# Performance work log

Measured on AMD Instinct MI355X. Metric: run time of the kernel, lower is better.

The kernel has to match this reference:

```python
import jax, jax.numpy as jnp
import numpy as np

N = 500_000      # nodes
E = 4_000_000    # edges (avg degree 8)
F_IN = 24        # n_input (includeHeading=False, coords=False)
H = 64           # n_hidden
K = 6            # K_block Chebyshev order
OUT = 6          # n_output
EPS = 1e-5       # BatchNorm eps


def setup_inputs() -> dict:
    key = jax.random.key(0)
    ks = jax.random.split(key, 8)
    x = jax.random.normal(ks[0], (N, F_IN), dtype=jnp.float32)
    edge_index = jax.random.randint(ks[1], (2, E), 0, N, dtype=jnp.int32)
    # ChebConv(24 -> 64, K=6): stacked per-order weights [K, F_IN, H] + bias
    W1 = jax.random.normal(ks[2], (K, F_IN, H), dtype=jnp.float32) * (1.0 / np.sqrt(F_IN))
    b1 = jnp.zeros((H,), dtype=jnp.float32)
    # BatchNorm1d(64) affine params
    gamma = jnp.ones((H,), dtype=jnp.float32)
    beta = jnp.zeros((H,), dtype=jnp.float32)
    # conv_mix ChebConv(64 -> 6, K=1)
    Wmix = jax.random.normal(ks[3], (1, H, OUT), dtype=jnp.float32) * (1.0 / np.sqrt(H))
    bmix = jnp.zeros((OUT,), dtype=jnp.float32)
    return {"x": x, "edge_index": edge_index, "W1": W1, "b1": b1,
            "gamma": gamma, "beta": beta, "Wmix": Wmix, "bmix": bmix}


def cheb_conv(x, edge_index, W, b):
    """PyG ChebConv with normalization='sym', lambda_max=2.
    L_hat = L - I = -D^{-1/2} A D^{-1/2} (zero diagonal).
    """
    Kk = W.shape[0]
    row, col = edge_index[0], edge_index[1]  # messages flow row -> col
    deg = jax.ops.segment_sum(jnp.ones((E,), x.dtype), col, num_segments=N)
    dis = jnp.where(deg > 0, jax.lax.rsqrt(jnp.maximum(deg, 1.0)), 0.0)
    norm = -(dis[row] * dis[col])  # [E]

    def prop(h):  # h: [N, F] -> L_hat @ h via gather-scale-scatter
        return jax.ops.segment_sum(norm[:, None] * h[row], col, num_segments=N)

    Tx0 = x
    out = Tx0 @ W[0]
    if Kk > 1:
        Tx1 = prop(Tx0)
        out = out + Tx1 @ W[1]
        for k in range(2, Kk):
            Tx2 = 2.0 * prop(Tx1) - Tx0
            out = out + Tx2 @ W[k]
            Tx0, Tx1 = Tx1, Tx2
    return out + b


def reference(x, edge_index, W1, b1, gamma, beta, Wmix, bmix):
    # Kipfblock: ChebConv -> BatchNorm1d (batch stats) -> ReLU
    h = cheb_conv(x, edge_index, W1, b1)            # [N, H]
    mean = jnp.mean(h, axis=0)
    var = jnp.mean(jnp.square(h - mean), axis=0)    # biased var, as torch BN training
    h = (h - mean) * jax.lax.rsqrt(var + EPS) * gamma + beta
    h = jax.nn.relu(h)
    # conv_mix: ChebConv K=1 reduces to a dense linear (T_0 = x only)
    y = h @ Wmix[0] + bmix                          # [N, OUT]
    # F.dropout is identity in eval mode
    return y
```

## Files before the change

### kernel.cpp

```cpp
#include <hip/hip_runtime.h>
#include <hip/hip_fp16.h>

#define NN 500000
#define NE 4000000
#define FI 24
#define FH 64
#define KC 6
#define FO 6
#define BN_EPS 1e-5f

#define SLOTS 32
#define RH 32
#define NMT (NN / 16)
#define PASS_GRID 1024

#define EPT 8
#define CHUNK (256 * EPT)
#define NCHUNK ((NE + CHUNK - 1) / CHUNK)

#define BUCKETS 512
#define BW 977
#define BCAP 15500

#define RMASK 0x7FFFFu

typedef _Float16 half8 __attribute__((ext_vector_type(8)));
typedef float f32x4 __attribute__((ext_vector_type(4)));
typedef int int4v __attribute__((ext_vector_type(4)));
union U4H8 { uint4 u; half8 h; };


__device__ __forceinline__ void acc8(float* a, float d, uint4 u) {
    const __half2* h2 = (const __half2*)&u;
    #pragma unroll
    for (int j = 0; j < 4; ++j) {
        float2 f = __half22float2(h2[j]);
        a[2 * j]     += d * f.x;
        a[2 * j + 1] += d * f.y;
    }
}

__device__ __forceinline__ uint4 pack8(const float* a) {
    uint4 u;
    __half2* h2 = (__half2*)&u;
    #pragma unroll
    for (int j = 0; j < 4; ++j) h2[j] = __floats2half2_rn(a[2 * j], a[2 * j + 1]);
    return u;
}


__global__ __launch_bounds__(256) void k_scatter(
    const int* __restrict__ row, const int* __restrict__ col,
    unsigned int* __restrict__ ebuf, int* __restrict__ cur) {
    __shared__ unsigned int val[CHUNK];
    __shared__ unsigned short bk[CHUNK];
    __shared__ int hist[BUCKETS], base[BUCKETS], rk[BUCKETS];
    for (int t = threadIdx.x; t < BUCKETS; t += 256) { hist[t] = 0; rk[t] = 0; }
    __syncthreads();
    const int b0 = blockIdx.x * CHUNK;
    #pragma unroll
    for (int i = 0; i < EPT / 4; ++i) {
        int li4 = (i * 256 + threadIdx.x) * 4;
        int e0 = b0 + li4;
        if (e0 + 4 <= NE) {
            int4v c4 = *(const int4v*)(col + e0);
            int4v r4 = *(const int4v*)(row + e0);
            #pragma unroll
            for (int j = 0; j < 4; ++j) {
                int c = c4[j], r = r4[j];
                int b = c / BW, cl = c - b * BW;
                val[li4 + j] = (unsigned int)r | ((unsigned int)cl << 19);
                bk[li4 + j] = (unsigned short)b;
                atomicAdd(&hist[b], 1);
            }
        } else {
            for (int j = 0; j < 4; ++j) {
                int e = e0 + j, li = li4 + j;
                if (e < NE) {
                    int c = col[e], r = row[e];
                    int b = c / BW, cl = c - b * BW;
                    val[li] = (unsigned int)r | ((unsigned int)cl << 19);
                    bk[li] = (unsigned short)b;
                    atomicAdd(&hist[b], 1);
                } else {
                    bk[li] = 0xFFFF;
                }
            }
        }
    }
    __syncthreads();
    for (int t = threadIdx.x; t < BUCKETS; t += 256) {
        int n = hist[t];
        base[t] = n ? atomicAdd(&cur[t], n) : 0;
    }
    __syncthreads();
    #pragma unroll
    for (int i = 0; i < EPT / 4; ++i) {
        int li4 = (i * 256 + threadIdx.x) * 4;
        #pragma unroll
        for (int j = 0; j < 4; ++j) {
            int li = li4 + j;
            int b = bk[li];
            if (b != 0xFFFF) {
                int rkk = atomicAdd(&rk[b], 1);
                int pos = base[b] + rkk;
                if (pos < BCAP) ebuf[(size_t)b * BCAP + pos] = val[li];
            }
        }
    }
}


__global__ __launch_bounds__(256) void k_build(
    const unsigned int* __restrict__ ebuf, const int* __restrict__ cur,
    int* __restrict__ cnt, int* __restrict__ csrcT) {
    __shared__ int cl_cnt[BW];
    const int b = blockIdx.x;
    const int nbase = b * BW;
    const int width = (NN - nbase < BW) ? (NN - nbase) : BW;
    for (int i = threadIdx.x; i < BW; i += 256) cl_cnt[i] = 0;
    __syncthreads();
    int nb = cur[b];
    if (nb > BCAP) nb = BCAP;
    for (int i = threadIdx.x; i < nb; i += 256) {
        unsigned int v = ebuf[(size_t)b * BCAP + i];
        int cl = v >> 19;
        int r = v & RMASK;
        int pos = atomicAdd(&cl_cnt[cl], 1);
        if (pos < SLOTS) csrcT[(size_t)pos * NN + nbase + cl] = r;
    }
    __syncthreads();
    for (int i = threadIdx.x; i < width; i += 256) cnt[nbase + i] = cl_cnt[i];
}

__global__ void k_dis(const int* __restrict__ cnt, float* __restrict__ dis) {
    int n = blockIdx.x * blockDim.x + threadIdx.x;
    if (n < NN) {
        int d = cnt[n];
        dis[n] = d > 0 ? rsqrtf((float)d) : 0.0f;
    }
}


__global__ __launch_bounds__(256) void k_pack(
    const int* __restrict__ cnt, unsigned int* __restrict__ csrcT) {
    int n = blockIdx.x * 256 + threadIdx.x;
    if (n >= NN) return;
    int deg = cnt[n];
    if (deg > SLOTS) deg = SLOTS;
    for (int s = 0; s < deg; ++s) {
        size_t idx = (size_t)s * NN + n;
        unsigned int r = csrcT[idx] & RMASK;
        int dg = cnt[r];
        if (dg > 8191) dg = 8191;
        csrcT[idx] = r | ((unsigned int)dg << 19);
    }
}


__global__ void k_xhalf(const float* __restrict__ x, __half* __restrict__ Th0) {
    int n = blockIdx.x * blockDim.x + threadIdx.x;
    if (n >= NN) return;
    const float* r = x + (size_t)n * FI;
    float v[24];
    #pragma unroll
    for (int i = 0; i < 6; ++i) {
        float4 f = ((const float4*)r)[i];
        v[4 * i] = f.x; v[4 * i + 1] = f.y; v[4 * i + 2] = f.z; v[4 * i + 3] = f.w;
    }
    uint4* o = (uint4*)(Th0 + (size_t)n * RH);
    o[0] = pack8(v); o[1] = pack8(v + 8); o[2] = pack8(v + 16);
    o[3] = make_uint4(0, 0, 0, 0);
}


template<bool FIRST>
__global__ __launch_bounds__(256) void k_prop(
    const int* __restrict__ cnt, const unsigned int* __restrict__ csrcT,
    const float* __restrict__ dis,
    const __half* __restrict__ Tin, const __half* __restrict__ Tpp,
    __half* __restrict__ Tout) {
    int t = blockIdx.x * 256 + threadIdx.x;
    int n = t >> 1, half = t & 1;
    if (n >= NN) return;
    int deg = cnt[n];
    if (deg > SLOTS) deg = SLOTS;
    float a[24];
    #pragma unroll
    for (int j = 0; j < 24; ++j) a[j] = 0.0f;
    int s = half;
    for (; s + 2 < deg; s += 4) {
        unsigned int e0 = csrcT[(size_t)s * NN + n];
        unsigned int e1 = csrcT[(size_t)(s + 2) * NN + n];
        const uint4* p0 = (const uint4*)(Tin + (size_t)(e0 & RMASK) * RH);
        const uint4* p1 = (const uint4*)(Tin + (size_t)(e1 & RMASK) * RH);
        uint4 u00 = p0[0], u01 = p0[1], u02 = p0[2];
        uint4 u10 = p1[0], u11 = p1[1], u12 = p1[2];
        unsigned int g0 = e0 >> 19, g1 = e1 >> 19;
        float d0 = g0 ? rsqrtf((float)g0) : 0.0f;
        float d1 = g1 ? rsqrtf((float)g1) : 0.0f;
        acc8(a, d0, u00); acc8(a + 8, d0, u01); acc8(a + 16, d0, u02);
        acc8(a, d1, u10); acc8(a + 8, d1, u11); acc8(a + 16, d1, u12);
    }
    if (s < deg) {
        unsigned int e0 = csrcT[(size_t)s * NN + n];
        unsigned int g0 = e0 >> 19;
        float d0 = g0 ? rsqrtf((float)g0) : 0.0f;
        const uint4* p0 = (const uint4*)(Tin + (size_t)(e0 & RMASK) * RH);
        acc8(a, d0, p0[0]); acc8(a + 8, d0, p0[1]); acc8(a + 16, d0, p0[2]);
    }
    #pragma unroll
    for (int j = 0; j < 24; ++j) a[j] += __shfl_xor(a[j], 1);
    float local[16];
    #pragma unroll
    for (int j = 0; j < 16; ++j) {
        float ev = a[j];
        float od = (j < 8) ? a[16 + j] : 0.0f;
        local[j] = half ? od : ev;
    }
    float m = FIRST ? -dis[n] : -2.0f * dis[n];
    if (FIRST) {
        #pragma unroll
        for (int j = 0; j < 16; ++j) local[j] *= m;
    } else {
        const uint4* pr = (const uint4*)(Tpp + (size_t)n * RH) + half * 2;
        uint4 q0 = pr[0], q1 = pr[1];
        float pv[16];
        {
            const __half2* h2 = (const __half2*)&q0;
            #pragma unroll
            for (int j = 0; j < 4; ++j) { float2 f = __half22float2(h2[j]); pv[2*j] = f.x; pv[2*j+1] = f.y; }
        }
        {
            const __half2* h2 = (const __half2*)&q1;
            #pragma unroll
            for (int j = 0; j < 4; ++j) { float2 f = __half22float2(h2[j]); pv[8+2*j] = f.x; pv[8+2*j+1] = f.y; }
        }
        #pragma unroll
        for (int j = 0; j < 16; ++j) local[j] = m * local[j] - pv[j];
    }
    uint4* o = (uint4*)(Tout + (size_t)n * RH) + half * 2;
    o[0] = pack8(local); o[1] = pack8(local + 8);
}


__device__ __forceinline__ void build_bfrags(const float* __restrict__ W1, uint4* Bf) {
    for (int s = threadIdx.x; s < KC * 4 * 64; s += 256) {
        int lane = s & 63, blk = s >> 6;
        int seg = blk >> 2, nb = blk & 3;
        int q = lane >> 4, n = lane & 15;
        float v[8];
        #pragma unroll
        for (int j = 0; j < 8; ++j) {
            int k = q * 8 + j;
            v[j] = (k < FI) ? W1[(seg * FI + k) * FH + nb * 16 + n] : 0.0f;
        }
        U4H8 u;
        __half2* h2 = (__half2*)&u;
        #pragma unroll
        for (int j = 0; j < 4; ++j) h2[j] = __floats2half2_rn(v[2 * j], v[2 * j + 1]);
        Bf[s] = u.u;
    }
}

__global__ __launch_bounds__(256) void k_pass1(
    const __half* __restrict__ Th, const float* __restrict__ W1,
    const float* __restrict__ b1, float* __restrict__ stats,
    __half* __restrict__ h) {
    __shared__ uint4 Bf[KC * 4 * 64];
    __shared__ float st[2 * FH];
    build_bfrags(W1, Bf);
    if (threadIdx.x < 2 * FH) st[threadIdx.x] = 0.0f;
    __syncthreads();
    const int lane = threadIdx.x & 63;
    const int q = lane >> 4, ln = lane & 15;
    const int wid = blockIdx.x * 4 + (threadIdx.x >> 6);
    const int nw = gridDim.x * 4;
    float bias[4];
    #pragma unroll
    for (int nb = 0; nb < 4; ++nb) bias[nb] = b1[nb * 16 + ln];
    float ssum[4] = {0, 0, 0, 0}, sqsum[4] = {0, 0, 0, 0};
    for (int t = wid; t < NMT; t += nw) {
        const int n0 = t * 16;
        f32x4 acc[4];
        #pragma unroll
        for (int nb = 0; nb < 4; ++nb)
            acc[nb] = (f32x4){bias[nb], bias[nb], bias[nb], bias[nb]};
        #pragma unroll
        for (int seg = 0; seg < KC; ++seg) {
            U4H8 a;
            a.u = *(const uint4*)(Th + (size_t)seg * ((size_t)NN * RH)
                                  + (size_t)(n0 + ln) * RH + q * 8);
            #pragma unroll
            for (int nb = 0; nb < 4; ++nb) {
                U4H8 b; b.u = Bf[(seg * 4 + nb) * 64 + lane];
                acc[nb] = __builtin_amdgcn_mfma_f32_16x16x32_f16(a.h, b.h, acc[nb], 0, 0, 0);
            }
        }
        #pragma unroll
        for (int nb = 0; nb < 4; ++nb) {
            #pragma unroll
            for (int r = 0; r < 4; ++r) {
                float v = acc[nb][r];
                ssum[nb] += v;
                sqsum[nb] += v * v;
                h[(size_t)(n0 + q * 4 + r) * FH + nb * 16 + ln] = __float2half(v);
            }
        }
    }
    #pragma unroll
    for (int nb = 0; nb < 4; ++nb) {
        ssum[nb]  += __shfl_xor(ssum[nb], 16);  ssum[nb]  += __shfl_xor(ssum[nb], 32);
        sqsum[nb] += __shfl_xor(sqsum[nb], 16); sqsum[nb] += __shfl_xor(sqsum[nb], 32);
    }
    if (lane < 16) {
        #pragma unroll
        for (int nb = 0; nb < 4; ++nb) {
            atomicAdd(&st[nb * 16 + ln], ssum[nb]);
            atomicAdd(&st[FH + nb * 16 + ln], sqsum[nb]);
        }
    }
    __syncthreads();
    if (threadIdx.x < 2 * FH) atomicAdd(&stats[threadIdx.x], st[threadIdx.x]);
}

__global__ void k_finalize(const float* __restrict__ stats, const float* __restrict__ gamma,
                           const float* __restrict__ beta, float* __restrict__ ss) {
    int f = threadIdx.x;
    if (f < FH) {
        float mean = stats[f] * (1.0f / NN);
        float var  = stats[f + FH] * (1.0f / NN) - mean * mean;
        float rstd = rsqrtf(var + BN_EPS);
        float sc = gamma[f] * rstd;
        ss[f] = sc;
        ss[f + FH] = beta[f] - mean * sc;
    }
}


__global__ __launch_bounds__(256) void k_pass2(
    const __half* __restrict__ h, const float* __restrict__ ss,
    const float* __restrict__ Wmix, const float* __restrict__ bmix,
    float* __restrict__ y) {
    __shared__ float tab[FH * 8];
    for (int f = threadIdx.x; f < FH; f += 256) {
        tab[f * 8 + 0] = ss[f];
        tab[f * 8 + 1] = ss[FH + f];
        #pragma unroll
        for (int o = 0; o < FO; ++o) tab[f * 8 + 2 + o] = Wmix[f * FO + o];
    }
    __syncthreads();
    int n = blockIdx.x * 256 + threadIdx.x;
    if (n >= NN) return;
    const uint4* hr = (const uint4*)(h + (size_t)n * FH);
    float p[FO];
    #pragma unroll
    for (int o = 0; o < FO; ++o) p[o] = bmix[o];
    #pragma unroll
    for (int blk = 0; blk < 8; ++blk) {
        U4H8 u; u.u = hr[blk];
        const __half2* h2 = (const __half2*)&u;
        #pragma unroll
        for (int j = 0; j < 4; ++j) {
            float2 f2 = __half22float2(h2[j]);
            int f = blk * 8 + j * 2;
            {
                float4 t0 = *(const float4*)&tab[f * 8];
                float4 t1 = *(const float4*)&tab[f * 8 + 4];
                float hv = fmaxf(f2.x * t0.x + t0.y, 0.0f);
                p[0] += hv * t0.z; p[1] += hv * t0.w;
                p[2] += hv * t1.x; p[3] += hv * t1.y;
                p[4] += hv * t1.z; p[5] += hv * t1.w;
            }
            {
                float4 t0 = *(const float4*)&tab[(f + 1) * 8];
                float4 t1 = *(const float4*)&tab[(f + 1) * 8 + 4];
                float hv = fmaxf(f2.y * t0.x + t0.y, 0.0f);
                p[0] += hv * t0.z; p[1] += hv * t0.w;
                p[2] += hv * t1.x; p[3] += hv * t1.y;
                p[4] += hv * t1.z; p[5] += hv * t1.w;
            }
        }
    }
    float* yo = y + (size_t)n * FO;
    #pragma unroll
    for (int o = 0; o < FO; ++o) yo[o] = p[o];
}


extern "C" void kernel_launch(void* const* d_in, const int* in_sizes, int n_in,
                              void* d_out, int out_size, void* d_ws, size_t ws_size,
                              hipStream_t stream) {
    const float* x     = (const float*)d_in[0];
    const int*   edge  = (const int*)d_in[1];
    const float* W1    = (const float*)d_in[2];
    const float* b1    = (const float*)d_in[3];
    const float* gamma = (const float*)d_in[4];
    const float* beta  = (const float*)d_in[5];
    const float* Wmix  = (const float*)d_in[6];
    const float* bmix  = (const float*)d_in[7];
    float* y = (float*)d_out;

    const int* row = edge;
    const int* col = edge + NE;

    const size_t O_CNT   = 0;
    const size_t O_DIS   = 500000;
    const size_t O_STATS = 1000000;
    const size_t O_SS    = 1000128;
    const size_t O_CSRC  = 1000256;
    const size_t O_TH    = 17000256;
    const size_t TOTAL_ELEMS = O_TH + 6ull * NN * RH / 2;
    if (ws_size < TOTAL_ELEMS * 4ull) return;

    float* wf = (float*)d_ws;
    int*   wi = (int*)d_ws;
    int*   cnt   = wi + O_CNT;
    float* dis   = wf + O_DIS;
    float* stats = wf + O_STATS;
    float* ss    = wf + O_SS;
    int*   csrcT = wi + O_CSRC;
    __half* hbuf = (__half*)(wi + O_CSRC);
    __half* Th   = (__half*)(wf + O_TH);
    __half* Th0  = Th;
    __half* Th1  = Th + 1ull * NN * RH;
    __half* Th2  = Th + 2ull * NN * RH;
    __half* Th3  = Th + 3ull * NN * RH;
    __half* Th4  = Th + 4ull * NN * RH;
    __half* Th5  = Th + 5ull * NN * RH;

    unsigned int* ebuf = (unsigned int*)Th5;
    int* cur = (int*)(ebuf + (size_t)BUCKETS * BCAP);

    (void)hipMemsetAsync(cur,   0, BUCKETS * sizeof(int), stream);
    (void)hipMemsetAsync(stats, 0, 128 * sizeof(float), stream);

    const int BS = 256;
    const int GN = (NN + BS - 1) / BS;
    const int GP = (2 * NN + BS - 1) / BS;

    k_scatter<<<NCHUNK, BS, 0, stream>>>(row, col, ebuf, cur);
    k_build<<<BUCKETS, BS, 0, stream>>>(ebuf, cur, cnt, csrcT);
    k_dis<<<GN, BS, 0, stream>>>(cnt, dis);
    k_pack<<<GN, BS, 0, stream>>>(cnt, (unsigned int*)csrcT);
    k_xhalf<<<GN, BS, 0, stream>>>(x, Th0);

    k_prop<true ><<<GP, BS, 0, stream>>>(cnt, (const unsigned int*)csrcT, dis, Th0, nullptr, Th1);
    k_prop<false><<<GP, BS, 0, stream>>>(cnt, (const unsigned int*)csrcT, dis, Th1, Th0, Th2);
    k_prop<false><<<GP, BS, 0, stream>>>(cnt, (const unsigned int*)csrcT, dis, Th2, Th1, Th3);
    k_prop<false><<<GP, BS, 0, stream>>>(cnt, (const unsigned int*)csrcT, dis, Th3, Th2, Th4);
    k_prop<false><<<GP, BS, 0, stream>>>(cnt, (const unsigned int*)csrcT, dis, Th4, Th3, Th5);

    k_pass1<<<PASS_GRID, 256, 0, stream>>>(Th, W1, b1, stats, hbuf);
    k_finalize<<<1, 64, 0, stream>>>(stats, gamma, beta, ss);
    k_pass2<<<GN, 256, 0, stream>>>(hbuf, ss, Wmix, bmix, y);
}
```

Baseline: 753.7 us.

## Fuse small preprocessing kernels and prefetch next tile in pass1

Folds the degree-normalization computation into k_build, merges k_pack and the x-to-half conversion into one k_prep kernel, and folds the BatchNorm finalize step into k_pass2, which removes three kernel launches. k_pass1 now software-pipelines its A-fragment loads by fetching the next tile's six segments while computing the current one. In exchange, pass1 uses more registers, which may lower occupancy, and every pass2 block recomputes the per-feature scale and shift.

```diff
diff --git a/kernel.cpp b/kernel.cpp
--- a/kernel.cpp
+++ b/kernel.cpp
@@ -113,7 +113,7 @@
 
 __global__ __launch_bounds__(256) void k_build(
     const unsigned int* __restrict__ ebuf, const int* __restrict__ cur,
-    int* __restrict__ cnt, int* __restrict__ csrcT) {
+    int* __restrict__ cnt, float* __restrict__ dis, int* __restrict__ csrcT) {
     __shared__ int cl_cnt[BW];
     const int b = blockIdx.x;
     const int nbase = b * BW;
@@ -130,20 +130,17 @@
         if (pos < SLOTS) csrcT[(size_t)pos * NN + nbase + cl] = r;
     }
     __syncthreads();
-    for (int i = threadIdx.x; i < width; i += 256) cnt[nbase + i] = cl_cnt[i];
-}
-
-__global__ void k_dis(const int* __restrict__ cnt, float* __restrict__ dis) {
-    int n = blockIdx.x * blockDim.x + threadIdx.x;
-    if (n < NN) {
-        int d = cnt[n];
-        dis[n] = d > 0 ? rsqrtf((float)d) : 0.0f;
-    }
-}
-
-
-__global__ __launch_bounds__(256) void k_pack(
-    const int* __restrict__ cnt, unsigned int* __restrict__ csrcT) {
+    for (int i = threadIdx.x; i < width; i += 256) {
+        int c = cl_cnt[i];
+        cnt[nbase + i] = c;
+        dis[nbase + i] = c > 0 ? rsqrtf((float)c) : 0.0f;
+    }
+}
+
+
+__global__ __launch_bounds__(256) void k_prep(
+    const int* __restrict__ cnt, unsigned int* __restrict__ csrcT,
+    const float* __restrict__ x, __half* __restrict__ Th0) {
     int n = blockIdx.x * 256 + threadIdx.x;
     if (n >= NN) return;
     int deg = cnt[n];
@@ -155,17 +152,11 @@
         if (dg > 8191) dg = 8191;
         csrcT[idx] = r | ((unsigned int)dg << 19);
     }
-}
-
-
-__global__ void k_xhalf(const float* __restrict__ x, __half* __restrict__ Th0) {
-    int n = blockIdx.x * blockDim.x + threadIdx.x;
-    if (n >= NN) return;
-    const float* r = x + (size_t)n * FI;
+    const float* xr = x + (size_t)n * FI;
     float v[24];
     #pragma unroll
     for (int i = 0; i < 6; ++i) {
-        float4 f = ((const float4*)r)[i];
+        float4 f = ((const float4*)xr)[i];
         v[4 * i] = f.x; v[4 * i + 1] = f.y; v[4 * i + 2] = f.z; v[4 * i + 3] = f.w;
     }
     uint4* o = (uint4*)(Th0 + (size_t)n * RH);
@@ -280,7 +271,25 @@
     #pragma unroll
     for (int nb = 0; nb < 4; ++nb) bias[nb] = b1[nb * 16 + ln];
     float ssum[4] = {0, 0, 0, 0}, sqsum[4] = {0, 0, 0, 0};
-    for (int t = wid; t < NMT; t += nw) {
+    int t = wid;
+    uint4 acur[KC];
+    if (t < NMT) {
+        #pragma unroll
+        for (int seg = 0; seg < KC; ++seg)
+            acur[seg] = *(const uint4*)(Th + (size_t)seg * ((size_t)NN * RH)
+                                        + (size_t)(t * 16 + ln) * RH + q * 8);
+    }
+    while (t < NMT) {
+        const int tn = t + nw;
+        uint4 anxt[KC];
+        #pragma unroll
+        for (int seg = 0; seg < KC; ++seg) anxt[seg] = acur[seg];
+        if (tn < NMT) {
+            #pragma unroll
+            for (int seg = 0; seg < KC; ++seg)
+                anxt[seg] = *(const uint4*)(Th + (size_t)seg * ((size_t)NN * RH)
+                                            + (size_t)(tn * 16 + ln) * RH + q * 8);
+        }
         const int n0 = t * 16;
         f32x4 acc[4];
         #pragma unroll
@@ -289,8 +298,7 @@
         #pragma unroll
         for (int seg = 0; seg < KC; ++seg) {
             U4H8 a;
-            a.u = *(const uint4*)(Th + (size_t)seg * ((size_t)NN * RH)
-                                  + (size_t)(n0 + ln) * RH + q * 8);
+            a.u = acur[seg];
             #pragma unroll
             for (int nb = 0; nb < 4; ++nb) {
                 U4H8 b; b.u = Bf[(seg * 4 + nb) * 64 + lane];
@@ -307,6 +315,9 @@
                 h[(size_t)(n0 + q * 4 + r) * FH + nb * 16 + ln] = __float2half(v);
             }
         }
+        #pragma unroll
+        for (int seg = 0; seg < KC; ++seg) acur[seg] = anxt[seg];
+        t = tn;
     }
     #pragma unroll
     for (int nb = 0; nb < 4; ++nb) {
@@ -324,28 +335,20 @@
     if (threadIdx.x < 2 * FH) atomicAdd(&stats[threadIdx.x], st[threadIdx.x]);
 }
 
-__global__ void k_finalize(const float* __restrict__ stats, const float* __restrict__ gamma,
-                           const float* __restrict__ beta, float* __restrict__ ss) {
-    int f = threadIdx.x;
-    if (f < FH) {
+
+__global__ __launch_bounds__(256) void k_pass2(
+    const __half* __restrict__ h, const float* __restrict__ stats,
+    const float* __restrict__ gamma, const float* __restrict__ beta,
+    const float* __restrict__ Wmix, const float* __restrict__ bmix,
+    float* __restrict__ y) {
+    __shared__ float tab[FH * 8];
+    for (int f = threadIdx.x; f < FH; f += 256) {
         float mean = stats[f] * (1.0f / NN);
         float var  = stats[f + FH] * (1.0f / NN) - mean * mean;
         float rstd = rsqrtf(var + BN_EPS);
         float sc = gamma[f] * rstd;
-        ss[f] = sc;
-        ss[f + FH] = beta[f] - mean * sc;
-    }
-}
-
-
-__global__ __launch_bounds__(256) void k_pass2(
-    const __half* __restrict__ h, const float* __restrict__ ss,
-    const float* __restrict__ Wmix, const float* __restrict__ bmix,
-    float* __restrict__ y) {
-    __shared__ float tab[FH * 8];
-    for (int f = threadIdx.x; f < FH; f += 256) {
-        tab[f * 8 + 0] = ss[f];
-        tab[f * 8 + 1] = ss[FH + f];
+        tab[f * 8 + 0] = sc;
+        tab[f * 8 + 1] = beta[f] - mean * sc;
         #pragma unroll
         for (int o = 0; o < FO; ++o) tab[f * 8 + 2 + o] = Wmix[f * FO + o];
     }
@@ -418,7 +421,6 @@
     int*   cnt   = wi + O_CNT;
     float* dis   = wf + O_DIS;
     float* stats = wf + O_STATS;
-    float* ss    = wf + O_SS;
     int*   csrcT = wi + O_CSRC;
     __half* hbuf = (__half*)(wi + O_CSRC);
     __half* Th   = (__half*)(wf + O_TH);
@@ -440,10 +442,8 @@
     const int GP = (2 * NN + BS - 1) / BS;
 
     k_scatter<<<NCHUNK, BS, 0, stream>>>(row, col, ebuf, cur);
-    k_build<<<BUCKETS, BS, 0, stream>>>(ebuf, cur, cnt, csrcT);
-    k_dis<<<GN, BS, 0, stream>>>(cnt, dis);
-    k_pack<<<GN, BS, 0, stream>>>(cnt, (unsigned int*)csrcT);
-    k_xhalf<<<GN, BS, 0, stream>>>(x, Th0);
+    k_build<<<BUCKETS, BS, 0, stream>>>(ebuf, cur, cnt, dis, csrcT);
+    k_prep<<<GN, BS, 0, stream>>>(cnt, (unsigned int*)csrcT, x, Th0);
 
     k_prop<true ><<<GP, BS, 0, stream>>>(cnt, (const unsigned int*)csrcT, dis, Th0, nullptr, Th1);
     k_prop<false><<<GP, BS, 0, stream>>>(cnt, (const unsigned int*)csrcT, dis, Th1, Th0, Th2);
@@ -452,6 +452,5 @@
     k_prop<false><<<GP, BS, 0, stream>>>(cnt, (const unsigned int*)csrcT, dis, Th4, Th3, Th5);
 
     k_pass1<<<PASS_GRID, 256, 0, stream>>>(Th, W1, b1, stats, hbuf);
-    k_finalize<<<1, 64, 0, stream>>>(stats, gamma, beta, ss);
-    k_pass2<<<GN, 256, 0, stream>>>(hbuf, ss, Wmix, bmix, y);
-}
+    k_pass2<<<GN, 256, 0, stream>>>(hbuf, stats, gamma, beta, Wmix, bmix, y);
+}
```

New measurement: 742.5 us. No clear change (-1.5%).
